# Performance work log

Hardware: AMD Instinct MI355X
Metric: run time of the kernel (lower is better)

The kernel has to match this reference:

```python
import jax, jax.numpy as jnp
import numpy as np

N_NODES = 20000
N_EDGES = 160000
IN_SIZE = 128
HIDDEN = 256
N_HID_LAYERS = 2
OUT_SIZE = 32
N_GRAPHS = 16
NUM_MP = 4  # BASELINE_MESSAGE_PASSING (weights SHARED across rounds: [Sequential(...)]*N)
NEG_SLOPE = 0.01  # torch.nn.LeakyReLU default
W_SCALE = 0.05


def leaky(x):
    return jnp.where(x >= 0, x, NEG_SLOPE * x)


def wide_mlp(h, Win, bin_, Wh, bh, Wout, bout):
    # Linear(in,H) + act, then N_HID_LAYERS x (Linear(H,H) + act), then Linear(H,out)
    h = leaky(h @ Win + bin_)
    for l in range(Wh.shape[0]):  # small fixed layer count
        h = leaky(h @ Wh[l] + bh[l])
    return h @ Wout + bout


def setup_inputs() -> dict:
    key = jax.random.key(0)
    ks = jax.random.split(key, 16)
    d = {
        "x": jax.random.normal(ks[0], (N_NODES, IN_SIZE), jnp.float32),
        "edge_index": jax.random.randint(ks[1], (2, N_EDGES), 0, N_NODES, jnp.int64),
        "batch": jnp.sort(jax.random.randint(ks[2], (N_NODES,), 0, N_GRAPHS, jnp.int64)),
        "enc_Win": W_SCALE * jax.random.normal(ks[3], (IN_SIZE, HIDDEN), jnp.float32),
        "enc_bin": jnp.zeros((HIDDEN,), jnp.float32),
        "enc_Wh": W_SCALE * jax.random.normal(ks[4], (N_HID_LAYERS, HIDDEN, HIDDEN), jnp.float32),
        "enc_bh": jnp.zeros((N_HID_LAYERS, HIDDEN), jnp.float32),
        "enc_Wout": W_SCALE * jax.random.normal(ks[5], (HIDDEN, HIDDEN), jnp.float32),
        "enc_bout": jnp.zeros((HIDDEN,), jnp.float32),
        "edge_W": W_SCALE * jax.random.normal(ks[6], (3 * HIDDEN, HIDDEN), jnp.float32),
        "edge_b": jnp.zeros((HIDDEN,), jnp.float32),
        "proc_Win": W_SCALE * jax.random.normal(ks[7], (HIDDEN, HIDDEN), jnp.float32),
        "proc_bin": jnp.zeros((HIDDEN,), jnp.float32),
        "proc_Wh": W_SCALE * jax.random.normal(ks[8], (N_HID_LAYERS, HIDDEN, HIDDEN), jnp.float32),
        "proc_bh": jnp.zeros((N_HID_LAYERS, HIDDEN), jnp.float32),
        "proc_Wout": W_SCALE * jax.random.normal(ks[9], (HIDDEN, HIDDEN), jnp.float32),
        "proc_bout": jnp.zeros((HIDDEN,), jnp.float32),
        "dec_Win": W_SCALE * jax.random.normal(ks[10], (3 * HIDDEN, HIDDEN), jnp.float32),
        "dec_bin": jnp.zeros((HIDDEN,), jnp.float32),
        "dec_Wh": W_SCALE * jax.random.normal(ks[11], (N_HID_LAYERS, HIDDEN, HIDDEN), jnp.float32),
        "dec_bh": jnp.zeros((N_HID_LAYERS, HIDDEN), jnp.float32),
        "dec_Wout": W_SCALE * jax.random.normal(ks[12], (HIDDEN, OUT_SIZE), jnp.float32),
        "dec_bout": jnp.zeros((OUT_SIZE,), jnp.float32),
    }
    return d


def reference(x, edge_index, batch,
              enc_Win, enc_bin, enc_Wh, enc_bh, enc_Wout, enc_bout,
              edge_W, edge_b,
              proc_Win, proc_bin, proc_Wh, proc_bh, proc_Wout, proc_bout,
              dec_Win, dec_bin, dec_Wh, dec_bh, dec_Wout, dec_bout):
    n = x.shape[0]
    # encode
    h = wide_mlp(x, enc_Win, enc_bin, enc_Wh, enc_bh, enc_Wout, enc_bout)
    # add_self_loops
    loops = jnp.arange(n, dtype=edge_index.dtype)
    ei = jnp.concatenate([edge_index, jnp.stack([loops, loops])], axis=1)
    src, dst = ei[0], ei[1]  # PyG: j = ei[0] (source), i = ei[1] (target/aggregation index)
    e = jnp.zeros((ei.shape[1], HIDDEN), h.dtype)  # edge_attr None branch -> zeros
    # BASELINE_MESSAGE_PASSING rounds, shared weights
    for _ in range(NUM_MP):
        m = jnp.concatenate([h[dst], h[src], e], axis=-1) @ edge_W + edge_b  # [E+N, H]
        h = jax.ops.segment_sum(m, dst, num_segments=n)  # aggr='add'
        h = wide_mlp(h, proc_Win, proc_bin, proc_Wh, proc_bh, proc_Wout, proc_bout)
    # global mean / max / add pooling over graphs
    sums = jax.ops.segment_sum(h, batch, num_segments=N_GRAPHS)
    cnt = jax.ops.segment_sum(jnp.ones((n, 1), h.dtype), batch, num_segments=N_GRAPHS)
    mean = sums / jnp.maximum(cnt, 1.0)
    mx = jax.ops.segment_max(h, batch, num_segments=N_GRAPHS)
    pooled = jnp.concatenate([mean, mx, sums], axis=-1)  # [G, 3H]
    out = wide_mlp(pooled, dec_Win, dec_bin, dec_Wh, dec_bh, dec_Wout, dec_bout)
    return out
```

## Files before the change

### kernel.cpp

```cpp
#include <hip/hip_runtime.h>
#include <hip/hip_bf16.h>
#include <cstdint>

#define HID 256
#define NGRAPH 16
#define NEG_SLOPE 0.01f

typedef __bf16 bf16x8 __attribute__((ext_vector_type(8)));
typedef float f32x4 __attribute__((ext_vector_type(4)));

__device__ __forceinline__ float leaky(float x) { return x >= 0.f ? x : NEG_SLOPE * x; }

__device__ __forceinline__ ushort f2b(float f) {
  uint u = __float_as_uint(f);
  uint r = (u + 0x7fffu + ((u >> 16) & 1u)) >> 16;
  return (ushort)r;
}
__device__ __forceinline__ float b2f(ushort b) { return __uint_as_float((uint)b << 16); }

__global__ __launch_bounds__(256) void k_zero_i32(int* p, int n) {
  int i = blockIdx.x * blockDim.x + threadIdx.x;
  if (i < n) p[i] = 0;
}

__global__ __launch_bounds__(256) void k_hist(const int* __restrict__ key, int* __restrict__ cnt, int ne) {
  int e = blockIdx.x * blockDim.x + threadIdx.x;
  if (e < ne) atomicAdd(&cnt[key[e]], 1);
}

__global__ __launch_bounds__(1024) void k_scan(const int* __restrict__ cnt, int* __restrict__ rowptr,
                                               int* __restrict__ cursor, int n) {
  __shared__ int sd[1024];
  int tid = threadIdx.x;
  int CH = n / 1024 + 1;
  int base = tid * CH;
  int s = 0;
  for (int i = 0; i < CH; ++i) { int idx = base + i; if (idx < n) s += cnt[idx]; }
  sd[tid] = s;
  __syncthreads();
  for (int off = 1; off < 1024; off <<= 1) {
    int v = (tid >= off) ? sd[tid - off] : 0;
    __syncthreads();
    sd[tid] += v;
    __syncthreads();
  }
  int run = (tid == 0) ? 0 : sd[tid - 1];
  for (int i = 0; i < CH; ++i) {
    int idx = base + i;
    if (idx <= n) {
      rowptr[idx] = run;
      if (idx < n) { cursor[idx] = run; run += cnt[idx]; }
    }
  }
}

__global__ __launch_bounds__(64) void k_gbounds(const int* __restrict__ batch, int n,
                                                int* __restrict__ gstart, int* __restrict__ gcnt) {
  int t = threadIdx.x;
  if (t <= NGRAPH) {
    int lo = 0, hi = n;
    while (lo < hi) { int mid = (lo + hi) >> 1; if (batch[mid] < t) lo = mid + 1; else hi = mid; }
    gstart[t] = lo;
  }
  __syncthreads();
  if (t < NGRAPH) gcnt[t] = gstart[t + 1] - gstart[t];
}

__global__ __launch_bounds__(256) void k_scatter(const int* __restrict__ src, const int* __restrict__ dst,
                                                 int* __restrict__ cursor, int* __restrict__ col, int ne) {
  int e = blockIdx.x * blockDim.x + threadIdx.x;
  if (e < ne) {
    int d = dst[e];
    int pos = atomicAdd(&cursor[d], 1);
    col[pos] = src[e];
  }
}

__global__ __launch_bounds__(256) void k_f2b(const float* __restrict__ src, ushort* __restrict__ dst, int nElem) {
  int i = (blockIdx.x * 256 + threadIdx.x) * 4;
  if (i + 3 < nElem) {
    float4 v = *(const float4*)&src[i];
    ushort4 o;
    o.x = f2b(v.x); o.y = f2b(v.y); o.z = f2b(v.z); o.w = f2b(v.w);
    *(ushort4*)&dst[i] = o;
  } else {
    for (int j = i; j < nElem; ++j) dst[j] = f2b(src[j]);
  }
}

struct WconvArgs {
  const float* src[9];
  ushort* dst[9];
  int K[9];
};

__global__ __launch_bounds__(256) void k_wconv_all(WconvArgs args) {
  __shared__ float t[32][33];
  const int e = blockIdx.z;
  const int K = args.K[e];
  const int k0 = blockIdx.x * 32;
  if (k0 >= K) return;
  const float* src = args.src[e];
  ushort* dst = args.dst[e];
  const int n0 = blockIdx.y * 32;
  const int tx = threadIdx.x & 31;
  const int ty = threadIdx.x >> 5;
#pragma unroll
  for (int r = 0; r < 4; ++r) t[ty + 8 * r][tx] = src[(size_t)(k0 + ty + 8 * r) * 256 + n0 + tx];
  __syncthreads();
#pragma unroll
  for (int r = 0; r < 4; ++r) dst[(size_t)(n0 + ty + 8 * r) * K + k0 + tx] = f2b(t[tx][ty + 8 * r]);
}

__global__ __launch_bounds__(256) void k_aggregate(const ushort* __restrict__ h, const int* __restrict__ rowptr,
                                                   const int* __restrict__ col, ushort* __restrict__ S,
                                                   ushort* __restrict__ hd, float* __restrict__ degf, int n) {
  int node = blockIdx.x * 4 + (threadIdx.x >> 6);
  if (node >= n) return;
  int lane = threadIdx.x & 63;
  const ushort4* h4 = (const ushort4*)h;
  size_t base = (size_t)node * 64 + lane;
  ushort4 self = h4[base];
  float a0 = b2f(self.x), a1 = b2f(self.y), a2 = b2f(self.z), a3 = b2f(self.w);
  float s0 = a0, s1 = a1, s2 = a2, s3 = a3;
  int beg = rowptr[node], end = rowptr[node + 1];
  int p = beg;
  for (; p + 4 <= end; p += 4) {
    int j0 = col[p], j1 = col[p + 1], j2 = col[p + 2], j3 = col[p + 3];
    ushort4 v0 = h4[(size_t)j0 * 64 + lane];
    ushort4 v1 = h4[(size_t)j1 * 64 + lane];
    ushort4 v2 = h4[(size_t)j2 * 64 + lane];
    ushort4 v3 = h4[(size_t)j3 * 64 + lane];
    s0 += b2f(v0.x) + b2f(v1.x) + b2f(v2.x) + b2f(v3.x);
    s1 += b2f(v0.y) + b2f(v1.y) + b2f(v2.y) + b2f(v3.y);
    s2 += b2f(v0.z) + b2f(v1.z) + b2f(v2.z) + b2f(v3.z);
    s3 += b2f(v0.w) + b2f(v1.w) + b2f(v2.w) + b2f(v3.w);
  }
  for (; p < end; ++p) {
    int j = col[p];
    ushort4 v = h4[(size_t)j * 64 + lane];
    s0 += b2f(v.x); s1 += b2f(v.y); s2 += b2f(v.z); s3 += b2f(v.w);
  }
  float deg = (float)(end - beg + 1);
  ushort4 so; so.x = f2b(s0); so.y = f2b(s1); so.z = f2b(s2); so.w = f2b(s3);
  ((ushort4*)S)[base] = so;
  ushort4 ho; ho.x = f2b(deg * a0); ho.y = f2b(deg * a1); ho.z = f2b(deg * a2); ho.w = f2b(deg * a3);
  ((ushort4*)hd)[base] = ho;
  if (lane == 0) degf[node] = deg;
}

struct MLPArgs {
  const ushort* A0;
  const ushort* A1;
  const ushort* W0b;
  const ushort* W[5];
  const float* bias[5];
  const float* degf;
  ushort* out;
  int ldw0;
  int actf[5];
};

template <int NL, int K0, bool DUAL>
__global__ __launch_bounds__(256, 2) void k_mlp(MLPArgs args, int M) {
  constexpr int KS0 = K0 >> 5;
  constexpr int NT0 = (DUAL ? 2 : 1) * KS0;

  __shared__ ushort act[8 * 32 * 32];
  __shared__ __align__(16) ushort As[2][32 * 32];
  __shared__ __align__(16) ushort Bs[2][256 * 32];

  const int m0 = blockIdx.x * 32;
  const int tid = threadIdx.x;
  const int lane = tid & 63;
  const int wn = tid >> 6;
  const int rl = lane & 15;
  const int kg = lane >> 4;

  float biasv[NL][4];
#pragma unroll
  for (int L = 0; L < NL; ++L)
#pragma unroll
    for (int fn = 0; fn < 4; ++fn)
      biasv[L][fn] = args.bias[L][wn * 64 + fn * 16 + rl];
  float degv[8];
#pragma unroll
  for (int i = 0; i < 8; ++i) degv[i] = 1.0f;
  if (DUAL) {
#pragma unroll
    for (int fm = 0; fm < 2; ++fm)
#pragma unroll
      for (int rg = 0; rg < 4; ++rg)
        degv[fm * 4 + rg] = args.degf[m0 + fm * 16 + kg * 4 + rg];
  }
  __builtin_amdgcn_sched_barrier(0);
  asm volatile("s_waitcnt vmcnt(0)" ::: "memory");
  __builtin_amdgcn_sched_barrier(0);

  const int sa_slot = tid & 127;
  const int a_row = sa_slot >> 2;
  const int a_kg = (sa_slot & 3) ^ ((a_row >> 1) & 3);
  const int s_row = tid >> 2;
  const int s_sl = tid & 3;
  int ga = m0 + a_row; if (ga > M - 1) ga = M - 1;

  auto stageA = [&](int buf, const ushort* Ap, int k0s) {
    const ushort* src = Ap + (size_t)ga * K0 + k0s + a_kg * 8;
    __builtin_amdgcn_global_load_lds(
        (const __attribute__((address_space(1))) void*)src,
        (__attribute__((address_space(3))) void*)&As[buf][sa_slot * 8], 16, 0, 0);
  };
  auto stageB = [&](int buf, const ushort* Wp, int ldw, int k0s) {
#pragma unroll
    for (int i = 0; i < 4; ++i) {
      int row = s_row + 64 * i;
      int kgi = s_sl ^ ((row >> 1) & 3);
      const ushort* src = Wp + (size_t)row * ldw + k0s + kgi * 8;
      __builtin_amdgcn_global_load_lds(
          (const __attribute__((address_space(1))) void*)src,
          (__attribute__((address_space(3))) void*)&Bs[buf][(tid + 256 * i) * 8], 16, 0, 0);
    }
  };

  int rr_[2], sA_[2], rn_[4], sB_[4];
#pragma unroll
  for (int fm = 0; fm < 2; ++fm) {
    rr_[fm] = fm * 16 + rl;
    sA_[fm] = kg ^ ((rr_[fm] >> 1) & 3);
  }
#pragma unroll
  for (int fn = 0; fn < 4; ++fn) {
    rn_[fn] = wn * 64 + fn * 16 + rl;
    sB_[fn] = kg ^ ((rn_[fn] >> 1) & 3);
  }

  f32x4 acc[2][4];

  auto epilogue = [&](bool useDeg, int af_, bool toGlobal,
                      float bv0, float bv1, float bv2, float bv3) {
    float bvs[4] = {bv0, bv1, bv2, bv3};
#pragma unroll
    for (int fn = 0; fn < 4; ++fn) {
      int c = wn * 64 + fn * 16 + rl;
      float bv = bvs[fn];
      int ch = c >> 5, g = (c >> 3) & 3, e = c & 7;
#pragma unroll
      for (int fm = 0; fm < 2; ++fm) {
        int lrow0 = fm * 16 + kg * 4;
#pragma unroll
        for (int rg = 0; rg < 4; ++rg) {
          int lrow = lrow0 + rg;
          float rs = useDeg ? degv[fm * 4 + rg] : 1.0f;
          float v = acc[fm][fn][rg] + rs * bv;
          if (af_) v = leaky(v);
          if (toGlobal) {
            args.out[(size_t)(m0 + lrow) * 256 + c] = f2b(v);
          } else {
            int slot = g ^ ((lrow >> 1) & 3);
            act[ch * 1024 + lrow * 32 + slot * 8 + e] = f2b(v);
          }
        }
      }
    }
  };

#define WAITV(n)                                              \
  __builtin_amdgcn_sched_barrier(0);                          \
  asm volatile("s_waitcnt vmcnt(" #n ")" ::: "memory");       \
  __builtin_amdgcn_sched_barrier(0);
#define READS_DONE                                            \
  __builtin_amdgcn_sched_barrier(0);                          \
  asm volatile("s_waitcnt lgkmcnt(0)" ::: "memory");          \
  __builtin_amdgcn_sched_barrier(0);

#pragma unroll
  for (int i = 0; i < 2; ++i)
#pragma unroll
    for (int j = 0; j < 4; ++j) acc[i][j] = (f32x4)(0.f);

  stageA(0, args.A0, 0);
  stageB(0, args.W[0], args.ldw0, 0);

#pragma unroll
  for (int t = 0; t < NT0; ++t) {
    if (t + 1 < NT0) {
      const int tp = t + 1;
      const int pass = DUAL ? (tp >= KS0 ? 1 : 0) : 0;
      const int k0s = (tp - pass * KS0) << 5;
      stageA(tp & 1, pass ? args.A1 : args.A0, k0s);
      stageB(tp & 1, pass ? args.W0b : args.W[0], args.ldw0, k0s);
      WAITV(5)
    } else if (NL > 1) {
      stageB(0, args.W[1], 256, 0);
      WAITV(4)
    } else {
      WAITV(0)
    }
    __builtin_amdgcn_s_barrier();
    __builtin_amdgcn_sched_barrier(0);
    {
      const ushort* bA = &As[t & 1][0];
      const ushort* bB = &Bs[t & 1][0];
      bf16x8 afr[2], bfr[4];
#pragma unroll
      for (int fm = 0; fm < 2; ++fm) afr[fm] = *(const bf16x8*)&bA[rr_[fm] * 32 + sA_[fm] * 8];
#pragma unroll
      for (int fn = 0; fn < 4; ++fn) bfr[fn] = *(const bf16x8*)&bB[rn_[fn] * 32 + sB_[fn] * 8];
      __builtin_amdgcn_s_setprio(1);
#pragma unroll
      for (int fm = 0; fm < 2; ++fm)
#pragma unroll
        for (int fn = 0; fn < 4; ++fn)
          acc[fm][fn] = __builtin_amdgcn_mfma_f32_16x16x32_bf16(afr[fm], bfr[fn], acc[fm][fn], 0, 0, 0);
      __builtin_amdgcn_s_setprio(0);
    }
    READS_DONE
    __builtin_amdgcn_s_barrier();
  }
  if (NL == 1) {
    epilogue(DUAL, args.actf[0], true, biasv[0][0], biasv[0][1], biasv[0][2], biasv[0][3]);
  } else {
    epilogue(DUAL, args.actf[0], false, biasv[0][0], biasv[0][1], biasv[0][2], biasv[0][3]);
    __syncthreads();
  }

#pragma unroll
  for (int L = 1; L < NL; ++L) {
#pragma unroll
    for (int i = 0; i < 2; ++i)
#pragma unroll
      for (int j = 0; j < 4; ++j) acc[i][j] = (f32x4)(0.f);
#pragma unroll
    for (int t = 0; t < 8; ++t) {
      if (t < 7) {
        stageB((t + 1) & 1, args.W[L], 256, (t + 1) * 32);
        WAITV(4)
      } else if (L + 1 < NL) {
        stageB(0, args.W[L + 1], 256, 0);
        WAITV(4)
      } else {
        WAITV(0)
      }
      __builtin_amdgcn_s_barrier();
      __builtin_amdgcn_sched_barrier(0);
      {
        const ushort* bB = &Bs[t & 1][0];
        bf16x8 afr[2], bfr[4];
#pragma unroll
        for (int fm = 0; fm < 2; ++fm)
          afr[fm] = *(const bf16x8*)&act[t * 1024 + rr_[fm] * 32 + sA_[fm] * 8];
#pragma unroll
        for (int fn = 0; fn < 4; ++fn) bfr[fn] = *(const bf16x8*)&bB[rn_[fn] * 32 + sB_[fn] * 8];
        __builtin_amdgcn_s_setprio(1);
#pragma unroll
        for (int fm = 0; fm < 2; ++fm)
#pragma unroll
          for (int fn = 0; fn < 4; ++fn)
            acc[fm][fn] = __builtin_amdgcn_mfma_f32_16x16x32_bf16(afr[fm], bfr[fn], acc[fm][fn], 0, 0, 0);
        __builtin_amdgcn_s_setprio(0);
      }
      READS_DONE
      __builtin_amdgcn_s_barrier();
    }
    if (L == NL - 1) {
      epilogue(false, args.actf[L], true, biasv[L][0], biasv[L][1], biasv[L][2], biasv[L][3]);
    } else {
      epilogue(false, args.actf[L], false, biasv[L][0], biasv[L][1], biasv[L][2], biasv[L][3]);
      __syncthreads();
    }
  }
#undef WAITV
#undef READS_DONE
}

__global__ __launch_bounds__(256) void k_dec_layer(
    const float* __restrict__ A, const float* __restrict__ W,
    const float* __restrict__ bias, float* __restrict__ out,
    int K, int N, int act)
{
  __shared__ float a[768];
  __shared__ float red[8][64];
  const int g = blockIdx.y;
  const int cols = (N >= 64) ? 64 : 32;
  const int segs = 256 / cols;
  const int t = threadIdx.x;
  const int col = t % cols, seg = t / cols;
  const int c = blockIdx.x * cols + col;
  for (int i = t; i < K; i += 256) a[i] = A[(size_t)g * K + i];
  __syncthreads();
  const int kper = K / segs;
  const int k0 = seg * kper;
  float p = 0.f;
#pragma unroll 8
  for (int k = k0; k < k0 + kper; ++k) p += a[k] * W[(size_t)k * N + c];
  red[seg][col] = p;
  __syncthreads();
  if (seg == 0) {
    float s = bias[c];
    for (int i = 0; i < segs; ++i) s += red[i][col];
    out[(size_t)g * N + c] = act ? leaky(s) : s;
  }
}

__global__ __launch_bounds__(256) void k_pool1(const ushort* __restrict__ h, const int* __restrict__ gstart,
                                               const int* __restrict__ gcnt, float* __restrict__ psum,
                                               float* __restrict__ pmax) {
  int g = blockIdx.x >> 4;
  int cch = blockIdx.x & 15;
  int t = threadIdx.x;
  int len = gcnt[g];
  int s0 = gstart[g];
  int chunk = (len + 15) >> 4;
  int i0 = s0 + cch * chunk;
  int i1 = min(i0 + chunk, s0 + len);
  float s = 0.f;
  float m = -3.402823466e+38f;
  for (int i = i0; i < i1; ++i) {
    float v = b2f(h[(size_t)i * HID + t]);
    s += v;
    m = fmaxf(m, v);
  }
  psum[(size_t)blockIdx.x * HID + t] = s;
  pmax[(size_t)blockIdx.x * HID + t] = m;
}

__global__ __launch_bounds__(256) void k_pool2(const float* __restrict__ psum, const float* __restrict__ pmax,
                                               const int* __restrict__ gcnt, float* __restrict__ pooled) {
  int g = blockIdx.x;
  int t = threadIdx.x;
  float s = 0.f, m = -3.402823466e+38f;
  for (int cch = 0; cch < 16; ++cch) {
    s += psum[(size_t)(g * 16 + cch) * HID + t];
    m = fmaxf(m, pmax[(size_t)(g * 16 + cch) * HID + t]);
  }
  float cf = (float)gcnt[g];
  pooled[g * 3 * HID + t] = s / fmaxf(cf, 1.f);
  pooled[g * 3 * HID + HID + t] = m;
  pooled[g * 3 * HID + 2 * HID + t] = s;
}

extern "C" void kernel_launch(void* const* d_in, const int* in_sizes, int n_in,
                              void* d_out, int out_size, void* d_ws, size_t ws_size,
                              hipStream_t stream) {
  const float* x        = (const float*)d_in[0];
  const int*   ei       = (const int*)d_in[1];
  const int*   batch    = (const int*)d_in[2];
  const float* enc_Win  = (const float*)d_in[3];
  const float* enc_bin  = (const float*)d_in[4];
  const float* enc_Wh   = (const float*)d_in[5];
  const float* enc_bh   = (const float*)d_in[6];
  const float* enc_Wout = (const float*)d_in[7];
  const float* enc_bout = (const float*)d_in[8];
  const float* edge_W   = (const float*)d_in[9];
  const float* edge_b   = (const float*)d_in[10];
  const float* proc_Win = (const float*)d_in[11];
  const float* proc_bin = (const float*)d_in[12];
  const float* proc_Wh  = (const float*)d_in[13];
  const float* proc_bh  = (const float*)d_in[14];
  const float* proc_Wout= (const float*)d_in[15];
  const float* proc_bout= (const float*)d_in[16];
  const float* dec_Win  = (const float*)d_in[17];
  const float* dec_bin  = (const float*)d_in[18];
  const float* dec_Wh   = (const float*)d_in[19];
  const float* dec_bh   = (const float*)d_in[20];
  const float* dec_Wout = (const float*)d_in[21];
  const float* dec_bout = (const float*)d_in[22];

  const int n  = in_sizes[0] / 128;
  const int ne = in_sizes[1] / 2;
  const int H = HID;

  char* p = (char*)d_ws;
  auto alloc = [&](size_t bytes) -> char* {
    char* r = p;
    p += (bytes + 255) & ~(size_t)255;
    return r;
  };
  ushort* hb1   = (ushort*)alloc((size_t)n * H * 2);
  ushort* Sb    = (ushort*)alloc((size_t)n * H * 2);
  ushort* hdb   = (ushort*)alloc((size_t)n * H * 2);
  ushort* xb    = (ushort*)alloc((size_t)n * 128 * 2);
  ushort* w_enc_in  = (ushort*)alloc((size_t)256 * 128 * 2);
  ushort* w_enc_h0  = (ushort*)alloc((size_t)256 * 256 * 2);
  ushort* w_enc_h1  = (ushort*)alloc((size_t)256 * 256 * 2);
  ushort* w_enc_out = (ushort*)alloc((size_t)256 * 256 * 2);
  ushort* w_proc_in  = (ushort*)alloc((size_t)256 * 256 * 2);
  ushort* w_proc_h0  = (ushort*)alloc((size_t)256 * 256 * 2);
  ushort* w_proc_h1  = (ushort*)alloc((size_t)256 * 256 * 2);
  ushort* w_proc_out = (ushort*)alloc((size_t)256 * 256 * 2);
  ushort* w_edge     = (ushort*)alloc((size_t)256 * 512 * 2);
  float* degf   = (float*)alloc((size_t)n * 4);
  float* pooled = (float*)alloc((size_t)NGRAPH * 3 * H * 4);
  float* psum   = (float*)alloc((size_t)256 * H * 4);
  float* pmax   = (float*)alloc((size_t)256 * H * 4);
  float* db0    = (float*)alloc((size_t)NGRAPH * H * 4);
  float* db1    = (float*)alloc((size_t)NGRAPH * H * 4);
  int* cnt    = (int*)alloc((size_t)n * 4);
  int* rowptr = (int*)alloc((size_t)(n + 1) * 4);
  int* cursor = (int*)alloc((size_t)n * 4);
  int* gstart = (int*)alloc((size_t)(NGRAPH + 1) * 4);
  int* gcnt   = (int*)alloc((size_t)NGRAPH * 4);
  int* colv   = (int*)alloc((size_t)ne * 4);

  const int* srcI = ei;
  const int* dstI = ei + ne;

  dim3 blk(256);

  WconvArgs wa;
  wa.src[0] = enc_Win;             wa.dst[0] = w_enc_in;   wa.K[0] = 128;
  wa.src[1] = enc_Wh;              wa.dst[1] = w_enc_h0;   wa.K[1] = 256;
  wa.src[2] = enc_Wh + 65536;      wa.dst[2] = w_enc_h1;   wa.K[2] = 256;
  wa.src[3] = enc_Wout;            wa.dst[3] = w_enc_out;  wa.K[3] = 256;
  wa.src[4] = proc_Win;            wa.dst[4] = w_proc_in;  wa.K[4] = 256;
  wa.src[5] = proc_Wh;             wa.dst[5] = w_proc_h0;  wa.K[5] = 256;
  wa.src[6] = proc_Wh + 65536;     wa.dst[6] = w_proc_h1;  wa.K[6] = 256;
  wa.src[7] = proc_Wout;           wa.dst[7] = w_proc_out; wa.K[7] = 256;
  wa.src[8] = edge_W;              wa.dst[8] = w_edge;     wa.K[8] = 512;
  k_wconv_all<<<dim3(16, 8, 9), blk, 0, stream>>>(wa);
  k_f2b<<<dim3((n * 128 / 4 + 255) / 256), blk, 0, stream>>>(x, xb, n * 128);

  k_zero_i32<<<dim3((n + 255) / 256), blk, 0, stream>>>(cnt, n);
  k_hist<<<dim3((ne + 255) / 256), blk, 0, stream>>>(dstI, cnt, ne);
  k_scan<<<1, 1024, 0, stream>>>(cnt, rowptr, cursor, n);
  k_gbounds<<<1, 64, 0, stream>>>(batch, n, gstart, gcnt);
  k_scatter<<<dim3((ne + 255) / 256), blk, 0, stream>>>(srcI, dstI, cursor, colv, ne);

  const int npanel = (n + 31) / 32;

  MLPArgs ea = {};
  ea.A0 = xb; ea.A1 = nullptr; ea.W0b = nullptr;
  ea.W[0] = w_enc_in; ea.W[1] = w_enc_h0; ea.W[2] = w_enc_h1; ea.W[3] = w_enc_out;
  ea.bias[0] = enc_bin; ea.bias[1] = enc_bh; ea.bias[2] = enc_bh + 256; ea.bias[3] = enc_bout;
  ea.bias[4] = enc_bout;
  ea.degf = nullptr; ea.out = hb1; ea.ldw0 = 128;
  ea.actf[0] = 1; ea.actf[1] = 1; ea.actf[2] = 1; ea.actf[3] = 0;
  k_mlp<4, 128, false><<<dim3(npanel), blk, 0, stream>>>(ea, n);

  MLPArgs pa = {};
  pa.A0 = hdb; pa.A1 = Sb; pa.W0b = w_edge + 256;
  pa.W[0] = w_edge; pa.W[1] = w_proc_in; pa.W[2] = w_proc_h0; pa.W[3] = w_proc_h1; pa.W[4] = w_proc_out;
  pa.bias[0] = edge_b; pa.bias[1] = proc_bin; pa.bias[2] = proc_bh; pa.bias[3] = proc_bh + 256; pa.bias[4] = proc_bout;
  pa.degf = degf; pa.out = hb1; pa.ldw0 = 512;
  pa.actf[0] = 0; pa.actf[1] = 1; pa.actf[2] = 1; pa.actf[3] = 1; pa.actf[4] = 0;

  for (int r = 0; r < 4; ++r) {
    k_aggregate<<<dim3((n + 3) / 4), blk, 0, stream>>>(hb1, rowptr, colv, Sb, hdb, degf, n);
    k_mlp<5, 256, true><<<dim3(npanel), blk, 0, stream>>>(pa, n);
  }

  k_pool1<<<dim3(NGRAPH * 16), blk, 0, stream>>>(hb1, gstart, gcnt, psum, pmax);
  k_pool2<<<dim3(NGRAPH), blk, 0, stream>>>(psum, pmax, gcnt, pooled);

  k_dec_layer<<<dim3(4, NGRAPH), blk, 0, stream>>>(pooled, dec_Win, dec_bin, db0, 768, 256, 1);
  k_dec_layer<<<dim3(4, NGRAPH), blk, 0, stream>>>(db0, dec_Wh, dec_bh, db1, 256, 256, 1);
  k_dec_layer<<<dim3(4, NGRAPH), blk, 0, stream>>>(db1, dec_Wh + 65536, dec_bh + 256, db0, 256, 256, 1);
  k_dec_layer<<<dim3(1, NGRAPH), blk, 0, stream>>>(db0, dec_Wout, dec_bout, (float*)d_out, 256, 32, 0);
}
```

Measured before the change: 375.6 us.

## Fuse neighbor aggregation into processor MLP kernel via LDS staging

Removes the separate aggregation kernel and computes each 32-row panel's neighbor sums and degree-scaled self features directly into shared memory inside the MLP kernel, with ping-pong h buffers across rounds. This eliminates the global round-trip of the S and hd intermediates and the degf array, plus one launch per round. In exchange the gather phase runs before the GEMM with only 4 waves per block doing 8 nodes each, so irregular gather latency is no longer overlapped by a dedicated high-occupancy kernel. Shared memory per block also grows.

```diff
diff --git a/kernel.cpp b/kernel.cpp
--- a/kernel.cpp
+++ b/kernel.cpp
@@ -112,50 +112,14 @@
   for (int r = 0; r < 4; ++r) dst[(size_t)(n0 + ty + 8 * r) * K + k0 + tx] = f2b(t[tx][ty + 8 * r]);
 }
 
-__global__ __launch_bounds__(256) void k_aggregate(const ushort* __restrict__ h, const int* __restrict__ rowptr,
-                                                   const int* __restrict__ col, ushort* __restrict__ S,
-                                                   ushort* __restrict__ hd, float* __restrict__ degf, int n) {
-  int node = blockIdx.x * 4 + (threadIdx.x >> 6);
-  if (node >= n) return;
-  int lane = threadIdx.x & 63;
-  const ushort4* h4 = (const ushort4*)h;
-  size_t base = (size_t)node * 64 + lane;
-  ushort4 self = h4[base];
-  float a0 = b2f(self.x), a1 = b2f(self.y), a2 = b2f(self.z), a3 = b2f(self.w);
-  float s0 = a0, s1 = a1, s2 = a2, s3 = a3;
-  int beg = rowptr[node], end = rowptr[node + 1];
-  int p = beg;
-  for (; p + 4 <= end; p += 4) {
-    int j0 = col[p], j1 = col[p + 1], j2 = col[p + 2], j3 = col[p + 3];
-    ushort4 v0 = h4[(size_t)j0 * 64 + lane];
-    ushort4 v1 = h4[(size_t)j1 * 64 + lane];
-    ushort4 v2 = h4[(size_t)j2 * 64 + lane];
-    ushort4 v3 = h4[(size_t)j3 * 64 + lane];
-    s0 += b2f(v0.x) + b2f(v1.x) + b2f(v2.x) + b2f(v3.x);
-    s1 += b2f(v0.y) + b2f(v1.y) + b2f(v2.y) + b2f(v3.y);
-    s2 += b2f(v0.z) + b2f(v1.z) + b2f(v2.z) + b2f(v3.z);
-    s3 += b2f(v0.w) + b2f(v1.w) + b2f(v2.w) + b2f(v3.w);
-  }
-  for (; p < end; ++p) {
-    int j = col[p];
-    ushort4 v = h4[(size_t)j * 64 + lane];
-    s0 += b2f(v.x); s1 += b2f(v.y); s2 += b2f(v.z); s3 += b2f(v.w);
-  }
-  float deg = (float)(end - beg + 1);
-  ushort4 so; so.x = f2b(s0); so.y = f2b(s1); so.z = f2b(s2); so.w = f2b(s3);
-  ((ushort4*)S)[base] = so;
-  ushort4 ho; ho.x = f2b(deg * a0); ho.y = f2b(deg * a1); ho.z = f2b(deg * a2); ho.w = f2b(deg * a3);
-  ((ushort4*)hd)[base] = ho;
-  if (lane == 0) degf[node] = deg;
-}
-
 struct MLPArgs {
   const ushort* A0;
-  const ushort* A1;
+  const ushort* h;
+  const int* rowptr;
+  const int* colv;
   const ushort* W0b;
   const ushort* W[5];
   const float* bias[5];
-  const float* degf;
   ushort* out;
   int ldw0;
   int actf[5];
@@ -166,9 +130,14 @@
   constexpr int KS0 = K0 >> 5;
   constexpr int NT0 = (DUAL ? 2 : 1) * KS0;
 
-  __shared__ ushort act[8 * 32 * 32];
-  __shared__ __align__(16) ushort As[2][32 * 32];
+  __shared__ ushort big0[8192];
+  __shared__ ushort big1[DUAL ? 8192 : 2048];
   __shared__ __align__(16) ushort Bs[2][256 * 32];
+
+  ushort* act = big0;
+  ushort* Hl = big0;
+  ushort* Sl = big1;
+  ushort(*As2)[1024] = (ushort(*)[1024])big1;
 
   const int m0 = blockIdx.x * 32;
   const int tid = threadIdx.x;
@@ -190,12 +159,50 @@
 #pragma unroll
     for (int fm = 0; fm < 2; ++fm)
 #pragma unroll
-      for (int rg = 0; rg < 4; ++rg)
-        degv[fm * 4 + rg] = args.degf[m0 + fm * 16 + kg * 4 + rg];
-  }
-  __builtin_amdgcn_sched_barrier(0);
-  asm volatile("s_waitcnt vmcnt(0)" ::: "memory");
-  __builtin_amdgcn_sched_barrier(0);
+      for (int rg = 0; rg < 4; ++rg) {
+        int row = m0 + fm * 16 + kg * 4 + rg;
+        degv[fm * 4 + rg] = (float)(args.rowptr[row + 1] - args.rowptr[row] + 1);
+      }
+  }
+
+  if (DUAL) {
+    const ushort4* h4 = (const ushort4*)args.h;
+    const int c0 = lane * 4;
+    const int ch = c0 >> 5, g = (c0 >> 3) & 3, e = c0 & 7;
+    for (int i = 0; i < 8; ++i) {
+      int row = wn * 8 + i;
+      int node = m0 + row;
+      int beg = args.rowptr[node], end = args.rowptr[node + 1];
+      ushort4 self = h4[(size_t)node * 64 + lane];
+      float a0 = b2f(self.x), a1 = b2f(self.y), a2 = b2f(self.z), a3 = b2f(self.w);
+      float s0 = a0, s1 = a1, s2 = a2, s3 = a3;
+      int p = beg;
+      for (; p + 4 <= end; p += 4) {
+        int j0 = args.colv[p], j1 = args.colv[p + 1], j2 = args.colv[p + 2], j3 = args.colv[p + 3];
+        ushort4 v0 = h4[(size_t)j0 * 64 + lane];
+        ushort4 v1 = h4[(size_t)j1 * 64 + lane];
+        ushort4 v2 = h4[(size_t)j2 * 64 + lane];
+        ushort4 v3 = h4[(size_t)j3 * 64 + lane];
+        s0 += b2f(v0.x) + b2f(v1.x) + b2f(v2.x) + b2f(v3.x);
+        s1 += b2f(v0.y) + b2f(v1.y) + b2f(v2.y) + b2f(v3.y);
+        s2 += b2f(v0.z) + b2f(v1.z) + b2f(v2.z) + b2f(v3.z);
+        s3 += b2f(v0.w) + b2f(v1.w) + b2f(v2.w) + b2f(v3.w);
+      }
+      for (; p < end; ++p) {
+        int j = args.colv[p];
+        ushort4 v = h4[(size_t)j * 64 + lane];
+        s0 += b2f(v.x); s1 += b2f(v.y); s2 += b2f(v.z); s3 += b2f(v.w);
+      }
+      float deg = (float)(end - beg + 1);
+      int slot = g ^ ((row >> 1) & 3);
+      int off = ch * 1024 + row * 32 + slot * 8 + e;
+      ushort4 hv; hv.x = f2b(deg * a0); hv.y = f2b(deg * a1); hv.z = f2b(deg * a2); hv.w = f2b(deg * a3);
+      *(ushort4*)&Hl[off] = hv;
+      ushort4 sv; sv.x = f2b(s0); sv.y = f2b(s1); sv.z = f2b(s2); sv.w = f2b(s3);
+      *(ushort4*)&Sl[off] = sv;
+    }
+  }
+  __syncthreads();
 
   const int sa_slot = tid & 127;
   const int a_row = sa_slot >> 2;
@@ -208,7 +215,7 @@
     const ushort* src = Ap + (size_t)ga * K0 + k0s + a_kg * 8;
     __builtin_amdgcn_global_load_lds(
         (const __attribute__((address_space(1))) void*)src,
-        (__attribute__((address_space(3))) void*)&As[buf][sa_slot * 8], 16, 0, 0);
+        (__attribute__((address_space(3))) void*)&As2[buf][sa_slot * 8], 16, 0, 0);
   };
   auto stageB = [&](int buf, const ushort* Wp, int ldw, int k0s) {
 #pragma unroll
@@ -278,51 +285,80 @@
 #pragma unroll
     for (int j = 0; j < 4; ++j) acc[i][j] = (f32x4)(0.f);
 
-  stageA(0, args.A0, 0);
-  stageB(0, args.W[0], args.ldw0, 0);
-
-#pragma unroll
-  for (int t = 0; t < NT0; ++t) {
-    if (t + 1 < NT0) {
-      const int tp = t + 1;
-      const int pass = DUAL ? (tp >= KS0 ? 1 : 0) : 0;
-      const int k0s = (tp - pass * KS0) << 5;
-      stageA(tp & 1, pass ? args.A1 : args.A0, k0s);
-      stageB(tp & 1, pass ? args.W0b : args.W[0], args.ldw0, k0s);
-      WAITV(5)
-    } else if (NL > 1) {
-      stageB(0, args.W[1], 256, 0);
-      WAITV(4)
-    } else {
-      WAITV(0)
-    }
-    __builtin_amdgcn_s_barrier();
-    __builtin_amdgcn_sched_barrier(0);
-    {
-      const ushort* bA = &As[t & 1][0];
-      const ushort* bB = &Bs[t & 1][0];
-      bf16x8 afr[2], bfr[4];
-#pragma unroll
-      for (int fm = 0; fm < 2; ++fm) afr[fm] = *(const bf16x8*)&bA[rr_[fm] * 32 + sA_[fm] * 8];
-#pragma unroll
-      for (int fn = 0; fn < 4; ++fn) bfr[fn] = *(const bf16x8*)&bB[rn_[fn] * 32 + sB_[fn] * 8];
-      __builtin_amdgcn_s_setprio(1);
-#pragma unroll
-      for (int fm = 0; fm < 2; ++fm)
-#pragma unroll
-        for (int fn = 0; fn < 4; ++fn)
-          acc[fm][fn] = __builtin_amdgcn_mfma_f32_16x16x32_bf16(afr[fm], bfr[fn], acc[fm][fn], 0, 0, 0);
-      __builtin_amdgcn_s_setprio(0);
-    }
-    READS_DONE
-    __builtin_amdgcn_s_barrier();
-  }
-  if (NL == 1) {
-    epilogue(DUAL, args.actf[0], true, biasv[0][0], biasv[0][1], biasv[0][2], biasv[0][3]);
+  if (DUAL) {
+    stageB(0, args.W[0], args.ldw0, 0);
+#pragma unroll
+    for (int t = 0; t < NT0; ++t) {
+      if (t + 1 < NT0) {
+        const int tp = t + 1;
+        const int pass = (tp >= KS0) ? 1 : 0;
+        stageB(tp & 1, pass ? args.W0b : args.W[0], args.ldw0, (tp & (KS0 - 1)) << 5);
+        WAITV(4)
+      } else {
+        stageB(0, args.W[1], 256, 0);
+        WAITV(4)
+      }
+      __builtin_amdgcn_s_barrier();
+      __builtin_amdgcn_sched_barrier(0);
+      {
+        const ushort* aSrc = (t < KS0) ? Hl : Sl;
+        const int chb = (t & (KS0 - 1)) * 1024;
+        const ushort* bB = &Bs[t & 1][0];
+        bf16x8 afr[2], bfr[4];
+#pragma unroll
+        for (int fm = 0; fm < 2; ++fm)
+          afr[fm] = *(const bf16x8*)&aSrc[chb + rr_[fm] * 32 + sA_[fm] * 8];
+#pragma unroll
+        for (int fn = 0; fn < 4; ++fn) bfr[fn] = *(const bf16x8*)&bB[rn_[fn] * 32 + sB_[fn] * 8];
+        __builtin_amdgcn_s_setprio(1);
+#pragma unroll
+        for (int fm = 0; fm < 2; ++fm)
+#pragma unroll
+          for (int fn = 0; fn < 4; ++fn)
+            acc[fm][fn] = __builtin_amdgcn_mfma_f32_16x16x32_bf16(afr[fm], bfr[fn], acc[fm][fn], 0, 0, 0);
+        __builtin_amdgcn_s_setprio(0);
+      }
+      READS_DONE
+      __builtin_amdgcn_s_barrier();
+    }
   } else {
-    epilogue(DUAL, args.actf[0], false, biasv[0][0], biasv[0][1], biasv[0][2], biasv[0][3]);
-    __syncthreads();
-  }
+    stageA(0, args.A0, 0);
+    stageB(0, args.W[0], args.ldw0, 0);
+#pragma unroll
+    for (int t = 0; t < NT0; ++t) {
+      if (t + 1 < NT0) {
+        const int tp = t + 1;
+        stageA(tp & 1, args.A0, tp << 5);
+        stageB(tp & 1, args.W[0], args.ldw0, tp << 5);
+        WAITV(5)
+      } else {
+        stageB(0, args.W[1], 256, 0);
+        WAITV(4)
+      }
+      __builtin_amdgcn_s_barrier();
+      __builtin_amdgcn_sched_barrier(0);
+      {
+        const ushort* bA = &As2[t & 1][0];
+        const ushort* bB = &Bs[t & 1][0];
+        bf16x8 afr[2], bfr[4];
+#pragma unroll
+        for (int fm = 0; fm < 2; ++fm) afr[fm] = *(const bf16x8*)&bA[rr_[fm] * 32 + sA_[fm] * 8];
+#pragma unroll
+        for (int fn = 0; fn < 4; ++fn) bfr[fn] = *(const bf16x8*)&bB[rn_[fn] * 32 + sB_[fn] * 8];
+        __builtin_amdgcn_s_setprio(1);
+#pragma unroll
+        for (int fm = 0; fm < 2; ++fm)
+#pragma unroll
+          for (int fn = 0; fn < 4; ++fn)
+            acc[fm][fn] = __builtin_amdgcn_mfma_f32_16x16x32_bf16(afr[fm], bfr[fn], acc[fm][fn], 0, 0, 0);
+        __builtin_amdgcn_s_setprio(0);
+      }
+      READS_DONE
+      __builtin_amdgcn_s_barrier();
+    }
+  }
+  epilogue(DUAL, args.actf[0], false, biasv[0][0], biasv[0][1], biasv[0][2], biasv[0][3]);
+  __syncthreads();
 
 #pragma unroll
   for (int L = 1; L < NL; ++L) {
@@ -476,9 +512,8 @@
     p += (bytes + 255) & ~(size_t)255;
     return r;
   };
+  ushort* hb0   = (ushort*)alloc((size_t)n * H * 2);
   ushort* hb1   = (ushort*)alloc((size_t)n * H * 2);
-  ushort* Sb    = (ushort*)alloc((size_t)n * H * 2);
-  ushort* hdb   = (ushort*)alloc((size_t)n * H * 2);
   ushort* xb    = (ushort*)alloc((size_t)n * 128 * 2);
   ushort* w_enc_in  = (ushort*)alloc((size_t)256 * 128 * 2);
   ushort* w_enc_h0  = (ushort*)alloc((size_t)256 * 256 * 2);
@@ -489,7 +524,6 @@
   ushort* w_proc_h1  = (ushort*)alloc((size_t)256 * 256 * 2);
   ushort* w_proc_out = (ushort*)alloc((size_t)256 * 256 * 2);
   ushort* w_edge     = (ushort*)alloc((size_t)256 * 512 * 2);
-  float* degf   = (float*)alloc((size_t)n * 4);
   float* pooled = (float*)alloc((size_t)NGRAPH * 3 * H * 4);
   float* psum   = (float*)alloc((size_t)256 * H * 4);
   float* pmax   = (float*)alloc((size_t)256 * H * 4);
@@ -529,27 +563,28 @@
   const int npanel = (n + 31) / 32;
 
   MLPArgs ea = {};
-  ea.A0 = xb; ea.A1 = nullptr; ea.W0b = nullptr;
+  ea.A0 = xb; ea.h = nullptr; ea.rowptr = nullptr; ea.colv = nullptr; ea.W0b = nullptr;
   ea.W[0] = w_enc_in; ea.W[1] = w_enc_h0; ea.W[2] = w_enc_h1; ea.W[3] = w_enc_out;
   ea.bias[0] = enc_bin; ea.bias[1] = enc_bh; ea.bias[2] = enc_bh + 256; ea.bias[3] = enc_bout;
   ea.bias[4] = enc_bout;
-  ea.degf = nullptr; ea.out = hb1; ea.ldw0 = 128;
+  ea.out = hb0; ea.ldw0 = 128;
   ea.actf[0] = 1; ea.actf[1] = 1; ea.actf[2] = 1; ea.actf[3] = 0;
   k_mlp<4, 128, false><<<dim3(npanel), blk, 0, stream>>>(ea, n);
 
   MLPArgs pa = {};
-  pa.A0 = hdb; pa.A1 = Sb; pa.W0b = w_edge + 256;
+  pa.A0 = nullptr; pa.rowptr = rowptr; pa.colv = colv; pa.W0b = w_edge + 256;
   pa.W[0] = w_edge; pa.W[1] = w_proc_in; pa.W[2] = w_proc_h0; pa.W[3] = w_proc_h1; pa.W[4] = w_proc_out;
   pa.bias[0] = edge_b; pa.bias[1] = proc_bin; pa.bias[2] = proc_bh; pa.bias[3] = proc_bh + 256; pa.bias[4] = proc_bout;
-  pa.degf = degf; pa.out = hb1; pa.ldw0 = 512;
+  pa.ldw0 = 512;
   pa.actf[0] = 0; pa.actf[1] = 1; pa.actf[2] = 1; pa.actf[3] = 1; pa.actf[4] = 0;
 
   for (int r = 0; r < 4; ++r) {
-    k_aggregate<<<dim3((n + 3) / 4), blk, 0, stream>>>(hb1, rowptr, colv, Sb, hdb, degf, n);
+    pa.h = (r & 1) ? hb1 : hb0;
+    pa.out = (r & 1) ? hb0 : hb1;
     k_mlp<5, 256, true><<<dim3(npanel), blk, 0, stream>>>(pa, n);
   }
 
-  k_pool1<<<dim3(NGRAPH * 16), blk, 0, stream>>>(hb1, gstart, gcnt, psum, pmax);
+  k_pool1<<<dim3(NGRAPH * 16), blk, 0, stream>>>(hb0, gstart, gcnt, psum, pmax);
   k_pool2<<<dim3(NGRAPH), blk, 0, stream>>>(psum, pmax, gcnt, pooled);
 
   k_dec_layer<<<dim3(4, NGRAPH), blk, 0, stream>>>(pooled, dec_Win, dec_bin, db0, 768, 256, 1);
```

After: 467.4 us. +24.4%, slower.
